# Kernel optimization log

Measured on AMD Instinct MI355X. Metric: run time of the kernel, lower is better.

## Reference

```python
import jax, jax.numpy as jnp
import numpy as np


def fwht(x):
    """Fast Walsh-Hadamard transform along last axis (n must be a power of 2).
    Loop runs log2(n) times (fixed, ~12 iters) -- fully vectorized butterflies."""
    n = x.shape[-1]
    prefix = x.shape[:-1]
    x = x.reshape(-1, n)
    h = 1
    while h < n:
        x = x.reshape(-1, n // (2 * h), 2, h)
        a, b = x[:, :, 0, :], x[:, :, 1, :]
        x = jnp.stack([a + b, a - b], axis=2).reshape(-1, n)
        h *= 2
    return x.reshape(prefix + (n,))


def setup_inputs() -> dict:
    key = jax.random.key(0)
    ks = jax.random.split(key, 8)
    Bz, S, N, M = 4, 2048, 4096, 4096   # batch, seq, in_features, out_features
    CODESZ, CB_SIZE, RANK = 8, 256, 64
    inp = {}
    inp["input"] = jax.random.normal(ks[0], (Bz, S, N), dtype=jnp.float32)
    inp["Qidxs"] = jax.random.randint(ks[1], (M, N // CODESZ), 0, CB_SIZE, dtype=jnp.int32)
    inp["codebook_vals"] = jax.random.normal(ks[2], (CB_SIZE, CODESZ), dtype=jnp.float32)
    # SU/SV are random sign vectors in QuIP#
    inp["SU"] = jnp.sign(jax.random.normal(ks[3], (N,), dtype=jnp.float32))
    inp["SV"] = jnp.sign(jax.random.normal(ks[4], (M,), dtype=jnp.float32))
    inp["Wscale"] = jnp.ones((), dtype=jnp.float32)
    inp["A"] = jax.random.normal(ks[5], (M, RANK), dtype=jnp.float32) * 0.01
    inp["B"] = jax.random.normal(ks[6], (RANK, N), dtype=jnp.float32) * 0.01
    return inp


def reference(input, Qidxs, codebook_vals, SU, SV, Wscale, A, B):
    n = SU.shape[0]   # in_features
    m = SV.shape[0]   # out_features
    lead = input.shape[:-1]
    x = input.reshape(-1, n).astype(jnp.float32)          # [T, n]
    # input rotation: x <- H^T (x * SU) / sqrt(n)   (matmul_hadUt, K=1 case)
    x = fwht(x * SU) * (1.0 / jnp.sqrt(jnp.float32(n)))
    # low-rank correction branch (rank > 0)
    Bx = x @ B.T                                          # [T, rank]
    # dequantize: codebook lookup [m, n/codesz, codesz] -> [m, n]
    W = codebook_vals[Qidxs].reshape(m, n)
    z = (x @ W.T) * Wscale                                # [T, m]
    z = z + Bx @ A.T
    # output rotation: z <- SV * (H z) / sqrt(m)
    z = fwht(z) * (1.0 / jnp.sqrt(jnp.float32(m))) * SV
    return z.reshape(lead + (m,))
```

## Files before the change

### kernel.cpp

```cpp
#include <hip/hip_runtime.h>
#include <hip/hip_bf16.h>


typedef __attribute__((ext_vector_type(8))) short short8;
typedef __attribute__((ext_vector_type(4))) float f32x4;

#define T_ROWS 8192
#define NDIM   4096
#define MDIM   4096
#define NT     (NDIM / 64)

__device__ __forceinline__ void gld_lds16(const void* g, void* lds_uniform) {
    __builtin_amdgcn_global_load_lds(
        (const __attribute__((address_space(1))) unsigned int*)(unsigned long long)(uintptr_t)g,
        (__attribute__((address_space(3))) unsigned int*)(unsigned int)(uintptr_t)lds_uniform,
        16, 0, 0);
}

#define FENCE asm volatile("" ::: "memory")
#define BAR   do { FENCE; __builtin_amdgcn_s_barrier(); FENCE; } while (0)
#define LGK0  do { asm volatile("s_waitcnt lgkmcnt(0)" ::: "memory"); \
                   __builtin_amdgcn_sched_barrier(0); } while (0)
#define VMC4  asm volatile("s_waitcnt vmcnt(4)" ::: "memory")
#define VMC0  asm volatile("s_waitcnt vmcnt(0)" ::: "memory")

__device__ __forceinline__ void bfly(float& a, float& b) {
    float s = a + b, d = a - b; a = s; b = d;
}
__device__ __forceinline__ void bfly4(float4& a, float4& b) {
    bfly(a.x, b.x); bfly(a.y, b.y); bfly(a.z, b.z); bfly(a.w, b.w);
}

__global__ __launch_bounds__(256) void fwht_in_kernel(
        const float* __restrict__ in, const float* __restrict__ SU,
        __hip_bfloat16* __restrict__ xout) {
    __shared__ float sh[4096];
    const int t = threadIdx.x;
    const size_t r = blockIdx.x;
    const float4* src = (const float4*)(in + (r << 12));
    const float4* su4 = (const float4*)SU;

    float4 v[4];
#pragma unroll
    for (int s = 0; s < 4; ++s) {
        float4 a = src[t + (s << 8)];
        float4 u = su4[t + (s << 8)];
        a.x *= u.x; a.y *= u.y; a.z *= u.z; a.w *= u.w;
        v[s] = a;
    }
#pragma unroll
    for (int s = 0; s < 4; ++s) {
        bfly(v[s].x, v[s].y); bfly(v[s].z, v[s].w);
        bfly(v[s].x, v[s].z); bfly(v[s].y, v[s].w);
    }
    bfly4(v[0], v[1]); bfly4(v[2], v[3]);
    bfly4(v[0], v[2]); bfly4(v[1], v[3]);

#pragma unroll
    for (int s = 0; s < 4; ++s) ((float4*)sh)[t + (s << 8)] = v[s];

#pragma unroll
    for (int h = 4; h <= 512; h <<= 1) {
        __syncthreads();
#pragma unroll
        for (int s = 0; s < 8; ++s) {
            int p = t + (s << 8);
            int i = ((p & ~(h - 1)) << 1) | (p & (h - 1));
            float a = sh[i], b = sh[i + h];
            sh[i] = a + b; sh[i + h] = a - b;
        }
    }
    __syncthreads();

    __hip_bfloat16* dst = xout + (r << 12);
    const float sc = 0.015625f;
#pragma unroll
    for (int s = 0; s < 4; ++s) {
        float4 a = ((const float4*)sh)[t + (s << 8)];
        union { __hip_bfloat16 h[4]; unsigned long long u; } pk;
        pk.h[0] = __float2bfloat16(a.x * sc);
        pk.h[1] = __float2bfloat16(a.y * sc);
        pk.h[2] = __float2bfloat16(a.z * sc);
        pk.h[3] = __float2bfloat16(a.w * sc);
        ((unsigned long long*)dst)[t + (s << 8)] = pk.u;
    }
}

__global__ __launch_bounds__(256) void dequant_kernel(
        const int* __restrict__ Qidxs, const float* __restrict__ cb,
        const float* __restrict__ Wscale, const float* __restrict__ A,
        const float* __restrict__ B, __hip_bfloat16* __restrict__ Weff) {
    __shared__ float At[64][68];
    __shared__ float Bs[64][68];
    __shared__ float cbs[2048];
    const int t = threadIdx.x;
    const int i0 = blockIdx.y * 64, j0 = blockIdx.x * 64;

    {
        const float* ga = A + (size_t)i0 * 64;
        const int r = t >> 2, kb = (t & 3) * 16;
#pragma unroll
        for (int j = 0; j < 16; ++j) At[kb + j][r] = ga[t * 16 + j];
        const int k = t >> 2, c0 = (t & 3) * 16;
        const float* gb = B + (size_t)k * NDIM + j0 + c0;
#pragma unroll
        for (int j = 0; j < 16; ++j) Bs[k][c0 + j] = gb[j];
#pragma unroll
        for (int j = 0; j < 8; ++j) cbs[t * 8 + j] = cb[t * 8 + j];
    }
    __syncthreads();

    const int ty = t >> 4, tx = t & 15;
    float acc[4][4];
#pragma unroll
    for (int a = 0; a < 4; ++a)
#pragma unroll
        for (int b = 0; b < 4; ++b) acc[a][b] = 0.f;

#pragma unroll 8
    for (int k = 0; k < 64; ++k) {
        const float4 av = *(const float4*)&At[k][ty * 4];
        const float4 bv = *(const float4*)&Bs[k][tx * 4];
        const float aa[4] = {av.x, av.y, av.z, av.w};
        const float bb[4] = {bv.x, bv.y, bv.z, bv.w};
#pragma unroll
        for (int ii = 0; ii < 4; ++ii)
#pragma unroll
            for (int jj = 0; jj < 4; ++jj) acc[ii][jj] += aa[ii] * bb[jj];
    }

    const float wsc = Wscale[0];
#pragma unroll
    for (int ii = 0; ii < 4; ++ii) {
        const int i = i0 + ty * 4 + ii;
        const int* qrow = Qidxs + (size_t)i * (NDIM / 8);
        union { __hip_bfloat16 h[4]; unsigned long long u; } pk;
#pragma unroll
        for (int jj = 0; jj < 4; ++jj) {
            const int j = j0 + tx * 4 + jj;
            const int idx = qrow[j >> 3];
            const float val = cbs[idx * 8 + (j & 7)] * wsc + acc[ii][jj];
            pk.h[jj] = __float2bfloat16(val);
        }
        *(unsigned long long*)&Weff[(size_t)i * NDIM + j0 + tx * 4] = pk.u;
    }
}

__global__ __launch_bounds__(512, 2) void gemm256_kernel(
        const __hip_bfloat16* __restrict__ X, const __hip_bfloat16* __restrict__ W,
        float* __restrict__ Z) {
    __shared__ short smem[65536];

    const int b = blockIdx.x;
    const int swz = (b & 7) * 64 + (b >> 3);
    const int bm = swz >> 4, bn = swz & 15;

    const int tid = threadIdx.x;
    const int lane = tid & 63, wid = tid >> 6;
    const int wm = wid >> 2, wn = wid & 3;
    const int lr = lane & 15, lk = lane >> 4;
    const int swb = (lr & 7) << 4;
    const int c0 = (((lk << 4)) ^ swb) >> 1;
    const int c1 = ((64 | (lk << 4)) ^ swb) >> 1;
    const int wbase = wid << 9;

    const int grow = tid >> 3;
    const int scol = (((tid & 7) ^ (grow & 7)) << 3);
    const __hip_bfloat16* gA = X + (size_t)(bm * 256 + grow) * NDIM + scol;
    const __hip_bfloat16* gB = W + (size_t)(bn * 256 + grow) * NDIM + scol;

#define LDSA(buf, h, q) (&smem[(buf) * 32768 + (h) * 8192 + (q) * 4096 + wbase])
#define LDSB(buf, h, q) (&smem[(buf) * 32768 + 16384 + (h) * 8192 + (q) * 4096 + wbase])
#define STA(kt, h, q) gld_lds16(gA + (size_t)((h) * 128 + (q) * 64) * NDIM + (kt) * 64, \
                                LDSA((kt) & 1, h, q))
#define STB(kt, h, q) gld_lds16(gB + (size_t)((h) * 128 + (q) * 64) * NDIM + (kt) * 64, \
                                LDSB((kt) & 1, h, q))

    f32x4 acc[8][4];
#pragma unroll
    for (int m = 0; m < 8; ++m)
#pragma unroll
        for (int n = 0; n < 4; ++n) acc[m][n] = 0.f;

    STA(0, 0, 0); STA(0, 0, 1); STA(0, 1, 0); STA(0, 1, 1);
    STB(0, 0, 0); STB(0, 0, 1); STB(0, 1, 0); STB(0, 1, 1);
    STB(1, 0, 0); STB(1, 0, 1); STB(1, 1, 0); STB(1, 1, 1);
    VMC4;
    BAR;

#define READ_A(M0) do { \
    aK0 = *(const short8*)&smem[aB + ((M0) * 16 + lr) * 64 + c0]; \
    aK1 = *(const short8*)&smem[aB + ((M0) * 16 + lr) * 64 + c1]; \
    bK0 = *(const short8*)&smem[aB + ((M0) * 16 + 16 + lr) * 64 + c0]; \
    bK1 = *(const short8*)&smem[aB + ((M0) * 16 + 16 + lr) * 64 + c1]; \
} while (0)

#define MFMA_PHASE(M0) do { \
    __builtin_amdgcn_s_setprio(1); \
    _Pragma("unroll") \
    for (int n = 0; n < 4; ++n) { \
        acc[M0][n]     = __builtin_amdgcn_mfma_f32_16x16x32_bf16(aK0, Bf[n][0], acc[M0][n], 0, 0, 0); \
        acc[M0][n]     = __builtin_amdgcn_mfma_f32_16x16x32_bf16(aK1, Bf[n][1], acc[M0][n], 0, 0, 0); \
        acc[M0 + 1][n] = __builtin_amdgcn_mfma_f32_16x16x32_bf16(bK0, Bf[n][0], acc[M0 + 1][n], 0, 0, 0); \
        acc[M0 + 1][n] = __builtin_amdgcn_mfma_f32_16x16x32_bf16(bK1, Bf[n][1], acc[M0 + 1][n], 0, 0, 0); \
    } \
    __builtin_amdgcn_s_setprio(0); \
    __builtin_amdgcn_sched_barrier(0); \
} while (0)

    for (int kt = 0; kt < NT; ++kt) {
        const int cur = (kt & 1) << 15;
        const int aB = cur + wm * 8192;
        const int bB = cur + 16384 + (wn >> 1) * 8192 + (wn & 1) * 4096;

        short8 Bf[4][2];
        short8 aK0, aK1, bK0, bK1;

#pragma unroll
        for (int n = 0; n < 4; ++n) {
            const int rb = (n * 16 + lr) * 64;
            Bf[n][0] = *(const short8*)&smem[bB + rb + c0];
            Bf[n][1] = *(const short8*)&smem[bB + rb + c1];
        }
        READ_A(0);
        if (kt + 1 < NT) { STA(kt + 1, 0, 0); STA(kt + 1, 0, 1); }
        BAR; LGK0;
        MFMA_PHASE(0);
        BAR;

        READ_A(2);
        if (kt + 1 < NT) { STA(kt + 1, 1, 0); STA(kt + 1, 1, 1); }
        BAR; LGK0;
        MFMA_PHASE(2);
        BAR;

        READ_A(4);
        if (kt + 2 < NT) { STB(kt + 2, 0, 0); STB(kt + 2, 0, 1); }
        BAR; LGK0;
        MFMA_PHASE(4);
        BAR;

        READ_A(6);
        if (kt + 2 < NT) { STB(kt + 2, 1, 0); STB(kt + 2, 1, 1); }
        BAR; LGK0;
        MFMA_PHASE(6);
        if (kt < NT - 2) { VMC4; } else { VMC0; }
        BAR;
    }

    const size_t r0 = (size_t)bm * 256 + wm * 128 + (lk << 2);
    const size_t cb0 = (size_t)bn * 256 + wn * 64 + lr;
#pragma unroll
    for (int m = 0; m < 8; ++m)
#pragma unroll
        for (int n = 0; n < 4; ++n) {
            const size_t col = cb0 + n * 16;
#pragma unroll
            for (int j = 0; j < 4; ++j)
                Z[(r0 + m * 16 + j) * MDIM + col] = acc[m][n][j];
        }
}

__global__ __launch_bounds__(256) void fwht_out_kernel(
        float* __restrict__ z, const float* __restrict__ SV) {
    __shared__ float sh[4096];
    const int t = threadIdx.x;
    const size_t r = blockIdx.x;
    float4* row = (float4*)(z + (r << 12));
    const float4* sv4 = (const float4*)SV;

    float4 v[4];
#pragma unroll
    for (int s = 0; s < 4; ++s) v[s] = row[t + (s << 8)];
#pragma unroll
    for (int s = 0; s < 4; ++s) {
        bfly(v[s].x, v[s].y); bfly(v[s].z, v[s].w);
        bfly(v[s].x, v[s].z); bfly(v[s].y, v[s].w);
    }
    bfly4(v[0], v[1]); bfly4(v[2], v[3]);
    bfly4(v[0], v[2]); bfly4(v[1], v[3]);

#pragma unroll
    for (int s = 0; s < 4; ++s) ((float4*)sh)[t + (s << 8)] = v[s];

#pragma unroll
    for (int h = 4; h <= 512; h <<= 1) {
        __syncthreads();
#pragma unroll
        for (int s = 0; s < 8; ++s) {
            int p = t + (s << 8);
            int i = ((p & ~(h - 1)) << 1) | (p & (h - 1));
            float a = sh[i], b = sh[i + h];
            sh[i] = a + b; sh[i + h] = a - b;
        }
    }
    __syncthreads();

    const float sc = 0.015625f;
#pragma unroll
    for (int s = 0; s < 4; ++s) {
        float4 a = ((const float4*)sh)[t + (s << 8)];
        float4 u = sv4[t + (s << 8)];
        a.x = a.x * sc * u.x; a.y = a.y * sc * u.y;
        a.z = a.z * sc * u.z; a.w = a.w * sc * u.w;
        row[t + (s << 8)] = a;
    }
}

extern "C" void kernel_launch(void* const* d_in, const int* in_sizes, int n_in,
                              void* d_out, int out_size, void* d_ws, size_t ws_size,
                              hipStream_t stream) {
    const float* input  = (const float*)d_in[0];
    const int*   Qidxs  = (const int*)d_in[1];
    const float* cbvals = (const float*)d_in[2];
    const float* SU     = (const float*)d_in[3];
    const float* SV     = (const float*)d_in[4];
    const float* Wscale = (const float*)d_in[5];
    const float* A      = (const float*)d_in[6];
    const float* B      = (const float*)d_in[7];
    float* out = (float*)d_out;

    __hip_bfloat16* xbf = (__hip_bfloat16*)d_ws;
    __hip_bfloat16* wbf = (__hip_bfloat16*)((char*)d_ws + (size_t)T_ROWS * NDIM * 2);

    fwht_in_kernel<<<T_ROWS, 256, 0, stream>>>(input, SU, xbf);
    dequant_kernel<<<dim3(MDIM / 64, MDIM / 64), 256, 0, stream>>>(
        Qidxs, cbvals, Wscale, A, B, wbf);
    gemm256_kernel<<<(T_ROWS / 256) * (MDIM / 256), 512, 0, stream>>>(xbf, wbf, out);
    fwht_out_kernel<<<T_ROWS, 256, 0, stream>>>(out, SV);
}
```

Before: 391.5 us.

## Restructure GEMM main loop with register double-buffered B fragments and fewer barriers

The bf16 MFMA GEMM main loop is rewritten so each K-tile issues its global-to-LDS prefetches up front. B fragments are double-buffered in registers across tiles and A fragment reads are interleaved with MFMA groups, using one barrier per tile instead of eight. The loop is manually unrolled by two with explicit vmcnt/lgkmcnt waits tuned per stage. This aims to cut barrier stalls and hide LDS latency behind MFMAs, at the cost of more registers and fragile hand-tuned wait counts that could race if wrong.

```diff
diff --git a/kernel.cpp b/kernel.cpp
--- a/kernel.cpp
+++ b/kernel.cpp
@@ -16,13 +16,6 @@
         (__attribute__((address_space(3))) unsigned int*)(unsigned int)(uintptr_t)lds_uniform,
         16, 0, 0);
 }
-
-#define FENCE asm volatile("" ::: "memory")
-#define BAR   do { FENCE; __builtin_amdgcn_s_barrier(); FENCE; } while (0)
-#define LGK0  do { asm volatile("s_waitcnt lgkmcnt(0)" ::: "memory"); \
-                   __builtin_amdgcn_sched_barrier(0); } while (0)
-#define VMC4  asm volatile("s_waitcnt vmcnt(4)" ::: "memory")
-#define VMC0  asm volatile("s_waitcnt vmcnt(0)" ::: "memory")
 
 __device__ __forceinline__ void bfly(float& a, float& b) {
     float s = a + b, d = a - b; a = s; b = d;
@@ -169,12 +162,69 @@
     const __hip_bfloat16* gA = X + (size_t)(bm * 256 + grow) * NDIM + scol;
     const __hip_bfloat16* gB = W + (size_t)(bn * 256 + grow) * NDIM + scol;
 
-#define LDSA(buf, h, q) (&smem[(buf) * 32768 + (h) * 8192 + (q) * 4096 + wbase])
-#define LDSB(buf, h, q) (&smem[(buf) * 32768 + 16384 + (h) * 8192 + (q) * 4096 + wbase])
-#define STA(kt, h, q) gld_lds16(gA + (size_t)((h) * 128 + (q) * 64) * NDIM + (kt) * 64, \
-                                LDSA((kt) & 1, h, q))
-#define STB(kt, h, q) gld_lds16(gB + (size_t)((h) * 128 + (q) * 64) * NDIM + (kt) * 64, \
-                                LDSB((kt) & 1, h, q))
+#define STA2(OFS, H, Q, BUF) gld_lds16(gA + (size_t)(((H) * 128 + (Q) * 64) * NDIM) + (OFS), \
+        &smem[(BUF) * 32768 + (H) * 8192 + (Q) * 4096 + wbase])
+#define STB2(OFS, H, Q, BUF) gld_lds16(gB + (size_t)(((H) * 128 + (Q) * 64) * NDIM) + (OFS), \
+        &smem[(BUF) * 32768 + 16384 + (H) * 8192 + (Q) * 4096 + wbase])
+#define STAGE_A(OFS, BUF) do { STA2(OFS,0,0,BUF); STA2(OFS,0,1,BUF); \
+                               STA2(OFS,1,0,BUF); STA2(OFS,1,1,BUF); } while (0)
+#define STAGE_B(OFS, BUF) do { STB2(OFS,0,0,BUF); STB2(OFS,0,1,BUF); \
+                               STB2(OFS,1,0,BUF); STB2(OFS,1,1,BUF); } while (0)
+
+#define RDA(D0, D1, D2, D3, M0, AB) do { \
+    D0 = *(const short8*)((AB) + ((M0) * 16 + lr) * 64 + c0); \
+    D1 = *(const short8*)((AB) + ((M0) * 16 + lr) * 64 + c1); \
+    D2 = *(const short8*)((AB) + ((M0) * 16 + 16 + lr) * 64 + c0); \
+    D3 = *(const short8*)((AB) + ((M0) * 16 + 16 + lr) * 64 + c1); \
+} while (0)
+
+#define RDB(BARR, BUF) do { \
+    const short* bB_ = smem + (BUF) * 32768 + 16384 + (wn * 64 + lr) * 64; \
+    _Pragma("unroll") \
+    for (int n = 0; n < 4; ++n) { \
+        BARR[2 * n]     = *(const short8*)(bB_ + n * 1024 + c0); \
+        BARR[2 * n + 1] = *(const short8*)(bB_ + n * 1024 + c1); \
+    } \
+} while (0)
+
+#define MFMA2(A0, A1, E0, E1, M0, BF) do { \
+    __builtin_amdgcn_s_setprio(1); \
+    _Pragma("unroll") \
+    for (int n = 0; n < 4; ++n) \
+        acc[M0][n] = __builtin_amdgcn_mfma_f32_16x16x32_bf16(A0, BF[2 * n], acc[M0][n], 0, 0, 0); \
+    _Pragma("unroll") \
+    for (int n = 0; n < 4; ++n) \
+        acc[(M0) + 1][n] = __builtin_amdgcn_mfma_f32_16x16x32_bf16(E0, BF[2 * n], acc[(M0) + 1][n], 0, 0, 0); \
+    _Pragma("unroll") \
+    for (int n = 0; n < 4; ++n) \
+        acc[M0][n] = __builtin_amdgcn_mfma_f32_16x16x32_bf16(A1, BF[2 * n + 1], acc[M0][n], 0, 0, 0); \
+    _Pragma("unroll") \
+    for (int n = 0; n < 4; ++n) \
+        acc[(M0) + 1][n] = __builtin_amdgcn_mfma_f32_16x16x32_bf16(E1, BF[2 * n + 1], acc[(M0) + 1][n], 0, 0, 0); \
+    __builtin_amdgcn_s_setprio(0); \
+} while (0)
+
+#define TILE(CUR, BF, BN, DO_STA, DO_STB, DO_BN, VMMID, VMEND, DO_ENDBAR) do { \
+    const short* aBase = smem + (CUR) * 32768 + wm * 8192; \
+    if (DO_STA) STAGE_A(64, 1 - (CUR)); \
+    if (DO_STB) STAGE_B(128, (CUR)); \
+    RDA(xa0, xa1, xb0, xb1, 0, aBase); \
+    RDA(ya0, ya1, yb0, yb1, 2, aBase); \
+    MFMA2(xa0, xa1, xb0, xb1, 0, BF); \
+    RDA(xa0, xa1, xb0, xb1, 4, aBase); \
+    MFMA2(ya0, ya1, yb0, yb1, 2, BF); \
+    RDA(ya0, ya1, yb0, yb1, 6, aBase); \
+    if (DO_BN) { \
+        asm volatile("s_waitcnt vmcnt(" #VMMID ")" ::: "memory"); \
+        RDB(BN, 1 - (CUR)); \
+    } \
+    MFMA2(xa0, xa1, xb0, xb1, 4, BF); \
+    MFMA2(ya0, ya1, yb0, yb1, 6, BF); \
+    asm volatile("s_waitcnt lgkmcnt(0)" ::: "memory"); \
+    asm volatile("s_waitcnt vmcnt(" #VMEND ")" ::: "memory"); \
+    if (DO_ENDBAR) __builtin_amdgcn_s_barrier(); \
+    gA += 64; gB += 64; \
+} while (0)
 
     f32x4 acc[8][4];
 #pragma unroll
@@ -182,71 +232,24 @@
 #pragma unroll
         for (int n = 0; n < 4; ++n) acc[m][n] = 0.f;
 
-    STA(0, 0, 0); STA(0, 0, 1); STA(0, 1, 0); STA(0, 1, 1);
-    STB(0, 0, 0); STB(0, 0, 1); STB(0, 1, 0); STB(0, 1, 1);
-    STB(1, 0, 0); STB(1, 0, 1); STB(1, 1, 0); STB(1, 1, 1);
-    VMC4;
-    BAR;
-
-#define READ_A(M0) do { \
-    aK0 = *(const short8*)&smem[aB + ((M0) * 16 + lr) * 64 + c0]; \
-    aK1 = *(const short8*)&smem[aB + ((M0) * 16 + lr) * 64 + c1]; \
-    bK0 = *(const short8*)&smem[aB + ((M0) * 16 + 16 + lr) * 64 + c0]; \
-    bK1 = *(const short8*)&smem[aB + ((M0) * 16 + 16 + lr) * 64 + c1]; \
-} while (0)
-
-#define MFMA_PHASE(M0) do { \
-    __builtin_amdgcn_s_setprio(1); \
-    _Pragma("unroll") \
-    for (int n = 0; n < 4; ++n) { \
-        acc[M0][n]     = __builtin_amdgcn_mfma_f32_16x16x32_bf16(aK0, Bf[n][0], acc[M0][n], 0, 0, 0); \
-        acc[M0][n]     = __builtin_amdgcn_mfma_f32_16x16x32_bf16(aK1, Bf[n][1], acc[M0][n], 0, 0, 0); \
-        acc[M0 + 1][n] = __builtin_amdgcn_mfma_f32_16x16x32_bf16(bK0, Bf[n][0], acc[M0 + 1][n], 0, 0, 0); \
-        acc[M0 + 1][n] = __builtin_amdgcn_mfma_f32_16x16x32_bf16(bK1, Bf[n][1], acc[M0 + 1][n], 0, 0, 0); \
-    } \
-    __builtin_amdgcn_s_setprio(0); \
-    __builtin_amdgcn_sched_barrier(0); \
-} while (0)
-
-    for (int kt = 0; kt < NT; ++kt) {
-        const int cur = (kt & 1) << 15;
-        const int aB = cur + wm * 8192;
-        const int bB = cur + 16384 + (wn >> 1) * 8192 + (wn & 1) * 4096;
-
-        short8 Bf[4][2];
-        short8 aK0, aK1, bK0, bK1;
-
-#pragma unroll
-        for (int n = 0; n < 4; ++n) {
-            const int rb = (n * 16 + lr) * 64;
-            Bf[n][0] = *(const short8*)&smem[bB + rb + c0];
-            Bf[n][1] = *(const short8*)&smem[bB + rb + c1];
-        }
-        READ_A(0);
-        if (kt + 1 < NT) { STA(kt + 1, 0, 0); STA(kt + 1, 0, 1); }
-        BAR; LGK0;
-        MFMA_PHASE(0);
-        BAR;
-
-        READ_A(2);
-        if (kt + 1 < NT) { STA(kt + 1, 1, 0); STA(kt + 1, 1, 1); }
-        BAR; LGK0;
-        MFMA_PHASE(2);
-        BAR;
-
-        READ_A(4);
-        if (kt + 2 < NT) { STB(kt + 2, 0, 0); STB(kt + 2, 0, 1); }
-        BAR; LGK0;
-        MFMA_PHASE(4);
-        BAR;
-
-        READ_A(6);
-        if (kt + 2 < NT) { STB(kt + 2, 1, 0); STB(kt + 2, 1, 1); }
-        BAR; LGK0;
-        MFMA_PHASE(6);
-        if (kt < NT - 2) { VMC4; } else { VMC0; }
-        BAR;
-    }
+    short8 B0r[8], B1r[8];
+    short8 xa0, xa1, xb0, xb1, ya0, ya1, yb0, yb1;
+
+    STAGE_A(0, 0);
+    STAGE_B(0, 0);
+    STAGE_B(64, 1);
+    asm volatile("s_waitcnt vmcnt(4)" ::: "memory");
+    __builtin_amdgcn_s_barrier();
+    RDB(B0r, 0);
+    asm volatile("s_waitcnt lgkmcnt(0)" ::: "memory");
+    __builtin_amdgcn_s_barrier();
+
+    for (int i = 0; i < 31; ++i) {
+        TILE(0, B0r, B1r, 1, 1, 1, 8, 4, 1);
+        TILE(1, B1r, B0r, 1, 1, 1, 8, 4, 1);
+    }
+    TILE(0, B0r, B1r, 1, 0, 1, 4, 0, 1);
+    TILE(1, B1r, B0r, 0, 0, 0, 0, 0, 0);
 
     const size_t r0 = (size_t)bm * 256 + wm * 128 + (lk << 2);
     const size_t cb0 = (size_t)bn * 256 + wn * 64 + lr;
```

Measured after the change: 385.5 us. Within noise of the previous version (-1.5%).
